# Kernel optimization log

Hardware: AMD Instinct MI355X
Metric: run time of the kernel (lower is better)

Reference implementation:

```python
import jax, jax.numpy as jnp
import numpy as np

B, S, D = 4, 2048, 512      # batch, seq_len, input_dim
E, H = 512, 8               # embed_dim, n_heads
HD = E // H                 # head_dim
ALPHA = 1.0                 # LRSA temperature


def setup_inputs() -> dict:
    key = jax.random.key(0)
    kx, kw1, kw2 = jax.random.split(key, 3)
    # xavier_uniform bounds for the two Linear layers (bias init is 0, as in module)
    b_qkv = float(np.sqrt(6.0 / (D + 3 * E)))
    b_o = float(np.sqrt(6.0 / (E + E)))
    return {
        "x": jax.random.normal(kx, (B, S, D), dtype=jnp.float32),
        "Wqkv": jax.random.uniform(kw1, (3 * E, D), jnp.float32, -b_qkv, b_qkv),
        "bqkv": jnp.zeros((3 * E,), jnp.float32),
        "Wo": jax.random.uniform(kw2, (E, E), jnp.float32, -b_o, b_o),
        "bo": jnp.zeros((E,), jnp.float32),
    }


def reference(x, Wqkv, bqkv, Wo, bo):
    Bx, Sx, _ = x.shape
    # QKV projection: [B,S,3E] -> [B,S,H,3*HD] -> [B,H,S,3*HD]
    qkv = (x @ Wqkv.T + bqkv).reshape(Bx, Sx, H, 3 * HD).transpose(0, 2, 1, 3)
    q, k, v = jnp.split(qkv, 3, axis=-1)  # each [B,H,S,HD]

    # LRSA: pairwise squared L2 distance logits ||q_i - k_j||^2
    q_norm2 = jnp.sum(q * q, axis=-1, keepdims=True)        # [B,H,S,1]
    k_norm2 = jnp.sum(k * k, axis=-1)[..., None, :]         # [B,H,1,S]
    qk = jnp.einsum("bhqd,bhkd->bhqk", q, k)                # [B,H,S,S]
    logits = q_norm2 - 2.0 * qk + k_norm2

    # global normalizers: frobenius norm of q, max per-token L2 norm of x
    fro_q = jnp.sqrt(jnp.sum(q * q))
    inf_2_x = jnp.max(jnp.sqrt(jnp.sum(x * x, axis=-1)))
    logits = logits / fro_q / inf_2_x

    attention = jax.nn.softmax(-ALPHA * logits, axis=-1)    # [B,H,S,S]
    values = jnp.einsum("bhqk,bhkd->bhqd", attention, v)    # [B,H,S,HD]
    values = values.transpose(0, 2, 1, 3).reshape(Bx, Sx, E)
    return values @ Wo.T + bo
```

## Files before the change

### kernel.cpp

```cpp
#include <hip/hip_runtime.h>
#include <hip/hip_bf16.h>
#include <math.h>

#define B_ 4
#define S_ 2048
#define D_ 512
#define E_ 512
#define H_ 8
#define HD_ 64
#define ALPHA_ 1.0f
#define M_ (B_*S_)
#define LOG2E_ 1.44269504088896340736f

typedef __attribute__((ext_vector_type(8))) short bf16x8;
typedef __attribute__((ext_vector_type(4))) float f32x4;

__device__ inline unsigned short f2bf(float f) {
    union { __hip_bfloat16 h; unsigned short u; } cv;
    cv.h = __float2bfloat16(f);
    return cv.u;
}
__device__ inline unsigned pack2bf(float a, float b) {
    union { __hip_bfloat162 h; unsigned u; } cv;
    cv.h = __float22bfloat162_rn(make_float2(a, b));
    return cv.u;
}
__device__ inline void gload16(const void* g, void* l) {
    __builtin_amdgcn_global_load_lds(
        (const __attribute__((address_space(1))) unsigned int*)g,
        (__attribute__((address_space(3))) unsigned int*)l, 16, 0, 0);
}
__device__ inline void gload4(const void* g, void* l) {
    __builtin_amdgcn_global_load_lds(
        (const __attribute__((address_space(1))) unsigned int*)g,
        (__attribute__((address_space(3))) unsigned int*)l, 4, 0, 0);
}

__global__ __launch_bounds__(256) void prep(const float* __restrict__ x,
                                            const float* __restrict__ Wqkv,
                                            const float* __restrict__ Wo,
                                            unsigned short* __restrict__ xbf,
                                            unsigned short* __restrict__ Wqkvb,
                                            unsigned short* __restrict__ Wob,
                                            float* __restrict__ xmax) {
    const int t   = threadIdx.x;
    const int bid = blockIdx.x;
    if (bid < 2048) {
        __shared__ float red[4];
        const int wid = t >> 6, lane = t & 63;
        const int row = bid * 4 + wid;
        const float* xr = &x[(size_t)row * D_ + lane * 8];
        const float4 a = *(const float4*)xr;
        const float4 b = *(const float4*)(xr + 4);
        float ss = a.x*a.x + a.y*a.y + a.z*a.z + a.w*a.w
                 + b.x*b.x + b.y*b.y + b.z*b.z + b.w*b.w;
        uint4 o;
        o.x = pack2bf(a.x, a.y); o.y = pack2bf(a.z, a.w);
        o.z = pack2bf(b.x, b.y); o.w = pack2bf(b.z, b.w);
        *(uint4*)&xbf[(size_t)row * D_ + lane * 8] = o;
        #pragma unroll
        for (int off = 32; off; off >>= 1) ss += __shfl_xor(ss, off);
        if (lane == 0) red[wid] = ss;
        __syncthreads();
        if (t == 0)
            xmax[bid] = fmaxf(fmaxf(red[0], red[1]), fmaxf(red[2], red[3]));
    } else {
        const int i  = (bid - 2048) * 256 + t;
        const int nq = 3 * E_ * D_ / 8;
        const float* src; unsigned short* dst; int j;
        if (i < nq) { src = Wqkv; dst = Wqkvb; j = i; }
        else        { src = Wo;   dst = Wob;   j = i - nq; }
        const float4 a = *(const float4*)&src[(size_t)j * 8];
        const float4 b = *(const float4*)&src[(size_t)j * 8 + 4];
        uint4 o;
        o.x = pack2bf(a.x, a.y); o.y = pack2bf(a.z, a.w);
        o.z = pack2bf(b.x, b.y); o.w = pack2bf(b.z, b.w);
        *(uint4*)&dst[(size_t)j * 8] = o;
    }
}

template<int N, int MODE>
__global__ __launch_bounds__(256) void gemm_mfma(const unsigned short* __restrict__ Abf,
                                                 const unsigned short* __restrict__ Wbf,
                                                 const float* __restrict__ bias,
                                                 void* __restrict__ out0,
                                                 void* __restrict__ out1,
                                                 void* __restrict__ out2,
                                                 float* __restrict__ part,
                                                 float* __restrict__ kn2) {
    __shared__ __align__(16) char At[16384];
    __shared__ __align__(16) char Wt[16384];

    const int t  = threadIdx.x;
    const int w  = t >> 6;
    const int l  = t & 63;
    const int g  = l >> 4;
    const int c  = l & 15;
    const int wm = w >> 1;
    const int wn = w & 1;
    const int m0 = blockIdx.y * 128;
    const int n0 = blockIdx.x * 128;

    f32x4 acc[4][4];
    #pragma unroll
    for (int i = 0; i < 4; ++i)
        #pragma unroll
        for (int j = 0; j < 4; ++j)
            #pragma unroll
            for (int r = 0; r < 4; ++r) acc[i][j][r] = 0.f;

    const int lr3 = l >> 3;
    const int colSwz = ((l & 7) * 16) ^ (lr3 << 4);
    const char* pA = (const char*)Abf + (size_t)(m0 + w * 8 + lr3) * 1024 + colSwz;
    const char* pB = (const char*)Wbf + (size_t)(n0 + w * 8 + lr3) * 1024 + colSwz;
    char* lA = At + w * 1024;
    char* lB = Wt + w * 1024;

    for (int k0 = 0; k0 < 512; k0 += 64) {
        __syncthreads();
        #pragma unroll
        for (int j = 0; j < 4; ++j) {
            gload16(pA + (size_t)j * 32768 + k0 * 2, lA + j * 4096);
            gload16(pB + (size_t)j * 32768 + k0 * 2, lB + j * 4096);
        }
        __syncthreads();

        bf16x8 af[4][2], wf[4][2];
        #pragma unroll
        for (int mt = 0; mt < 4; ++mt) {
            const int row = wm * 64 + mt * 16 + c;
            const int sw  = (row & 7) << 4;
            #pragma unroll
            for (int kc = 0; kc < 2; ++kc)
                af[mt][kc] = *(const bf16x8*)(At + row * 128 + (((kc * 4 + g) * 16) ^ sw));
        }
        #pragma unroll
        for (int nt = 0; nt < 4; ++nt) {
            const int row = wn * 64 + nt * 16 + c;
            const int sw  = (row & 7) << 4;
            #pragma unroll
            for (int kc = 0; kc < 2; ++kc)
                wf[nt][kc] = *(const bf16x8*)(Wt + row * 128 + (((kc * 4 + g) * 16) ^ sw));
        }
        #pragma unroll
        for (int mt = 0; mt < 4; ++mt)
            #pragma unroll
            for (int nt = 0; nt < 4; ++nt) {
                acc[mt][nt] = __builtin_amdgcn_mfma_f32_16x16x32_bf16(af[mt][0], wf[nt][0], acc[mt][nt], 0, 0, 0);
                acc[mt][nt] = __builtin_amdgcn_mfma_f32_16x16x32_bf16(af[mt][1], wf[nt][1], acc[mt][nt], 0, 0, 0);
            }
    }

    if (MODE == 1) {
        #pragma unroll
        for (int mt = 0; mt < 4; ++mt)
            #pragma unroll
            for (int reg = 0; reg < 4; ++reg) {
                const int m = m0 + wm * 64 + mt * 16 + g * 4 + reg;
                #pragma unroll
                for (int nt = 0; nt < 4; ++nt) {
                    const int n = n0 + wn * 64 + nt * 16 + c;
                    ((float*)out0)[(size_t)m * N + n] = acc[mt][nt][reg] + bias[n];
                }
            }
        return;
    }

    const int hb  = 2 * blockIdx.x + wn;
    const int cls = hb % 3;
    const int h   = hb / 3;
    const int b   = m0 >> 11;
    const int s0w = (m0 & 2047) + wm * 64;
    const size_t bhS = ((size_t)b * H_ + h) * S_;

    float kp[4][4];
    #pragma unroll
    for (int i = 0; i < 4; ++i)
        #pragma unroll
        for (int j = 0; j < 4; ++j) kp[i][j] = 0.f;

    if (cls == 2) {
        unsigned short* Vt_ = (unsigned short*)out2;
        #pragma unroll
        for (int nt = 0; nt < 4; ++nt) {
            const int n = n0 + wn * 64 + nt * 16 + c;
            const float bv = bias[n];
            const int d = nt * 16 + c;
            unsigned short* dbase = Vt_ + (((size_t)b * H_ + h) * HD_ + d) * S_ + s0w;
            #pragma unroll
            for (int mt = 0; mt < 4; ++mt) {
                uint2 pk;
                pk.x = pack2bf(acc[mt][nt][0] + bv, acc[mt][nt][1] + bv);
                pk.y = pack2bf(acc[mt][nt][2] + bv, acc[mt][nt][3] + bv);
                *(uint2*)&dbase[mt * 16 + g * 4] = pk;
            }
        }
    } else {
        unsigned short* dst0 = (cls == 0) ? (unsigned short*)out0 : (unsigned short*)out1;
        #pragma unroll
        for (int nt = 0; nt < 4; ++nt) {
            const int n = n0 + wn * 64 + nt * 16 + c;
            const float bv = bias[n];
            const int d = nt * 16 + c;
            #pragma unroll
            for (int mt = 0; mt < 4; ++mt)
                #pragma unroll
                for (int reg = 0; reg < 4; ++reg) {
                    const int s = s0w + mt * 16 + g * 4 + reg;
                    const float val = acc[mt][nt][reg] + bv;
                    kp[mt][reg] = fmaf(val, val, kp[mt][reg]);
                    dst0[(bhS + s) * HD_ + d] = f2bf(val);
                }
        }
    }

    __syncthreads();
    if (cls == 1) {
        float* scratch = (float*)At + wm * 1088;
        #pragma unroll
        for (int i = 0; i < 16; ++i) scratch[l * 17 + i] = kp[i >> 2][i & 3];
        asm volatile("s_waitcnt lgkmcnt(0)" ::: "memory");
        __builtin_amdgcn_sched_barrier(0);
        float sum = 0.f;
        #pragma unroll
        for (int cc = 0; cc < 16; ++cc)
            sum += scratch[(g * 16 + cc) * 17 + c];
        const int s = s0w + (c >> 2) * 16 + g * 4 + (c & 3);
        kn2[bhS + s] = sum;
    }
    __syncthreads();

    float qss = 0.f;
    if (cls == 0) {
        #pragma unroll
        for (int i = 0; i < 4; ++i)
            #pragma unroll
            for (int j = 0; j < 4; ++j) qss += kp[i][j];
    }
    float* red = (float*)At;
    red[t] = qss;
    __syncthreads();
    for (int s = 128; s; s >>= 1) {
        if (t < s) red[t] += red[t + s];
        __syncthreads();
    }
    if (t == 0) part[blockIdx.y * gridDim.x + blockIdx.x] = red[0];
}

__global__ __launch_bounds__(256) void finalize_scale(const float* __restrict__ part,
                                                      const float* __restrict__ xmax,
                                                      float* __restrict__ scal) {
    __shared__ float rs[256], rm[256];
    const int t = threadIdx.x;
    float ss = 0.f, mx = 0.f;
    for (int i = t; i < 768; i += 256) ss += part[i];
    for (int i = t; i < 2048; i += 256) mx = fmaxf(mx, xmax[i]);
    rs[t] = ss; rm[t] = mx;
    __syncthreads();
    for (int s = 128; s; s >>= 1) {
        if (t < s) { rs[t] += rs[t + s]; rm[t] = fmaxf(rm[t], rm[t + s]); }
        __syncthreads();
    }
    if (t == 0) scal[0] = ALPHA_ * LOG2E_ / (sqrtf(rs[0]) * sqrtf(rm[0]));
}

__global__ __launch_bounds__(512, 2) void attn_mfma(const unsigned short* __restrict__ Qb,
                                                    const unsigned short* __restrict__ Kb,
                                                    const unsigned short* __restrict__ Vtb,
                                                    const float* __restrict__ KN2,
                                                    const float* __restrict__ scal,
                                                    unsigned short* __restrict__ VALS) {
    __shared__ __align__(16) char lds[49664];
    char* Kl = lds;
    char* Vl = lds + 16384;
    char* Pl = lds + 32768;
    char* knl = lds + 49152;

    const int t  = threadIdx.x;
    const int w  = t >> 6;
    const int l  = t & 63;
    const int g  = l >> 4;
    const int c  = l & 15;
    const int bid  = blockIdx.y * gridDim.x + blockIdx.x;
    const int swid = (bid & 7) * 64 + (bid >> 3);
    const int bh = swid >> 4;
    const int qb = swid & 15;
    const float sc    = scal[0];
    const float ts2   = 2.0f * sc;
    const float nscal = -sc;

    const int qrow = qb * 128 + w * 16 + c;
    const size_t qoff = ((size_t)bh * S_ + qrow) * HD_;
    const bf16x8 qf0 = *(const bf16x8*)&Qb[qoff + g * 8];
    const bf16x8 qf1 = *(const bf16x8*)&Qb[qoff + 32 + g * 8];

    f32x4 acc[4];
    #pragma unroll
    for (int dt = 0; dt < 4; ++dt)
        #pragma unroll
        for (int r = 0; r < 4; ++r) acc[dt][r] = 0.f;
    float lpart = 0.f;

    const float* kn2g = &KN2[(size_t)bh * S_];
    char* Pw = Pl + w * 2048;
    const int swc = (c & 7) << 4;

    int offF[4][2];
    #pragma unroll
    for (int i = 0; i < 4; ++i) {
        offF[i][0] = (i * 16 + c) * 128 + ((g * 16) ^ swc);
        offF[i][1] = (i * 16 + c) * 128 + ((64 + g * 16) ^ swc);
    }
    int offPW[4];
    #pragma unroll
    for (int kt = 0; kt < 4; ++kt)
        offPW[kt] = c * 128 + ((kt * 32 + g * 8) ^ swc);
    const int offPA0 = c * 128 + ((g * 16) ^ swc);
    const int offPA1 = c * 128 + ((64 + g * 16) ^ swc);

    const int lr3 = l >> 3;
    const int colSwz = ((l & 7) * 16) ^ (lr3 << 4);
    const char* pK = (const char*)Kb + ((size_t)bh * S_ * HD_) * 2
                   + (size_t)(w * 8 + lr3) * 128 + colSwz;
    const char* pV = (const char*)Vtb + ((size_t)bh * HD_ * S_) * 2
                   + (size_t)(w * 8 + lr3) * (S_ * 2) + colSwz;
    char* lK = Kl + w * 1024;
    char* lV = Vl + w * 1024;

#define STAGE(T, buf) do {                                                    \
        gload16(pK + (size_t)(T) * 8192, lK + (buf) * 8192);                  \
        gload16(pV + (size_t)(T) * 128,  lV + (buf) * 8192);                  \
        if (w == 0) gload4(kn2g + (T) * 64 + l, knl + (buf) * 256);           \
    } while (0)

    auto compute_tile = [&](int cur) {
        const char* Kc = Kl + cur * 8192;
        const char* Vc = Vl + cur * 8192;
        const float* knc = (const float*)(knl + cur * 256);
        float sl[16];
        #pragma unroll
        for (int kt = 0; kt < 4; ++kt) {
            const bf16x8 ka0 = *(const bf16x8*)(Kc + offF[kt][0]);
            const bf16x8 ka1 = *(const bf16x8*)(Kc + offF[kt][1]);
            f32x4 sacc = {0.f, 0.f, 0.f, 0.f};
            sacc = __builtin_amdgcn_mfma_f32_16x16x32_bf16(ka0, qf0, sacc, 0, 0, 0);
            sacc = __builtin_amdgcn_mfma_f32_16x16x32_bf16(ka1, qf1, sacc, 0, 0, 0);
            const f32x4 kn4 = *(const f32x4*)&knc[kt * 16 + g * 4];
            #pragma unroll
            for (int rg = 0; rg < 4; ++rg)
                sl[kt * 4 + rg] = fmaf(sacc[rg], ts2, nscal * kn4[rg]);
        }

        float p[16];
        #pragma unroll
        for (int j = 0; j < 16; ++j) { p[j] = exp2f(sl[j]); lpart += p[j]; }

        #pragma unroll
        for (int kt = 0; kt < 4; ++kt) {
            uint2 pk;
            pk.x = pack2bf(p[kt * 4 + 0], p[kt * 4 + 1]);
            pk.y = pack2bf(p[kt * 4 + 2], p[kt * 4 + 3]);
            *(uint2*)(Pw + offPW[kt]) = pk;
        }
        asm volatile("s_waitcnt lgkmcnt(0)" ::: "memory");
        __builtin_amdgcn_sched_barrier(0);

        const bf16x8 pa0 = *(const bf16x8*)(Pw + offPA0);
        const bf16x8 pa1 = *(const bf16x8*)(Pw + offPA1);
        #pragma unroll
        for (int dt = 0; dt < 4; ++dt) {
            const bf16x8 vb0 = *(const bf16x8*)(Vc + offF[dt][0]);
            const bf16x8 vb1 = *(const bf16x8*)(Vc + offF[dt][1]);
            acc[dt] = __builtin_amdgcn_mfma_f32_16x16x32_bf16(pa0, vb0, acc[dt], 0, 0, 0);
            acc[dt] = __builtin_amdgcn_mfma_f32_16x16x32_bf16(pa1, vb1, acc[dt], 0, 0, 0);
        }
    };

    STAGE(0, 0);
    __syncthreads();
    for (int T = 0; T < 32; ++T) {
        const int cur = T & 1;
        if (T < 31) STAGE(T + 1, cur ^ 1);
        compute_tile(cur);
        __syncthreads();
    }
#undef STAGE

    lpart += __shfl_xor(lpart, 16);
    lpart += __shfl_xor(lpart, 32);

    const int b = bh >> 3, h = bh & 7;
    #pragma unroll
    for (int reg = 0; reg < 4; ++reg) {
        const float lq  = __shfl(lpart, g * 4 + reg);
        const float inv = 1.0f / lq;
        const int qg = qb * 128 + w * 16 + g * 4 + reg;
        unsigned short* dst = &VALS[((size_t)b * S_ + qg) * E_ + h * HD_];
        #pragma unroll
        for (int dt = 0; dt < 4; ++dt)
            dst[dt * 16 + c] = f2bf(acc[dt][reg] * inv);
    }
}

extern "C" void kernel_launch(void* const* d_in, const int* in_sizes, int n_in,
                              void* d_out, int out_size, void* d_ws, size_t ws_size,
                              hipStream_t stream) {
    const float* x    = (const float*)d_in[0];
    const float* Wqkv = (const float*)d_in[1];
    const float* bqkv = (const float*)d_in[2];
    const float* Wo   = (const float*)d_in[3];
    const float* bo   = (const float*)d_in[4];
    float* out = (float*)d_out;

    char* ws = (char*)d_ws;
    unsigned short* Qb    = (unsigned short*)(ws);
    unsigned short* Kb    = (unsigned short*)(ws + ((size_t) 8 << 20));
    unsigned short* Vtb   = (unsigned short*)(ws + ((size_t)16 << 20));
    unsigned short* VALb  = (unsigned short*)(ws + ((size_t)24 << 20));
    unsigned short* xbf   = (unsigned short*)(ws + ((size_t)32 << 20));
    unsigned short* Wqkvb = (unsigned short*)(ws + ((size_t)40 << 20));
    unsigned short* Wob   = (unsigned short*)(ws + ((size_t)42 << 20));
    float* KN2  = (float*)(ws + ((size_t)43 << 20));
    float* PART = (float*)(ws + ((size_t)43 << 20) + (256 << 10));
    float* XMAX = (float*)(ws + ((size_t)43 << 20) + (260 << 10));
    float* SCAL = (float*)(ws + ((size_t)43 << 20) + (272 << 10));

    prep<<<2560, 256, 0, stream>>>(x, Wqkv, Wo, xbf, Wqkvb, Wob, XMAX);

    gemm_mfma<3 * E_, 0><<<dim3(12, 64), 256, 0, stream>>>(xbf, Wqkvb, bqkv, Qb, Kb, Vtb, PART, KN2);

    finalize_scale<<<1, 256, 0, stream>>>(PART, XMAX, SCAL);

    attn_mfma<<<dim3(16, 32), 512, 0, stream>>>(Qb, Kb, Vtb, KN2, SCAL, VALb);

    gemm_mfma<E_, 1><<<dim3(4, 64), 256, 0, stream>>>(VALb, Wob, bo, out, nullptr, nullptr, nullptr, nullptr);
}
```

Before: 116.2 us.

## Double-buffer GEMM LDS tiles, fold scale finalize into attention, add MFMA priority

```diff
diff --git a/kernel.cpp b/kernel.cpp
--- a/kernel.cpp
+++ b/kernel.cpp
@@ -88,8 +88,8 @@
                                                  void* __restrict__ out2,
                                                  float* __restrict__ part,
                                                  float* __restrict__ kn2) {
-    __shared__ __align__(16) char At[16384];
-    __shared__ __align__(16) char Wt[16384];
+    __shared__ __align__(16) char At[2][16384];
+    __shared__ __align__(16) char Wt[2][16384];
 
     const int t  = threadIdx.x;
     const int w  = t >> 6;
@@ -113,17 +113,20 @@
     const int colSwz = ((l & 7) * 16) ^ (lr3 << 4);
     const char* pA = (const char*)Abf + (size_t)(m0 + w * 8 + lr3) * 1024 + colSwz;
     const char* pB = (const char*)Wbf + (size_t)(n0 + w * 8 + lr3) * 1024 + colSwz;
-    char* lA = At + w * 1024;
-    char* lB = Wt + w * 1024;
-
-    for (int k0 = 0; k0 < 512; k0 += 64) {
-        __syncthreads();
+
+    auto gstage = [&](int k0, int buf) {
         #pragma unroll
         for (int j = 0; j < 4; ++j) {
-            gload16(pA + (size_t)j * 32768 + k0 * 2, lA + j * 4096);
-            gload16(pB + (size_t)j * 32768 + k0 * 2, lB + j * 4096);
-        }
-        __syncthreads();
+            gload16(pA + (size_t)j * 32768 + (size_t)k0 * 2, At[buf] + w * 1024 + j * 4096);
+            gload16(pB + (size_t)j * 32768 + (size_t)k0 * 2, Wt[buf] + w * 1024 + j * 4096);
+        }
+    };
+
+    gstage(0, 0);
+    __syncthreads();
+    for (int i = 0; i < 8; ++i) {
+        const int buf = i & 1;
+        if (i < 7) gstage((i + 1) * 64, buf ^ 1);
 
         bf16x8 af[4][2], wf[4][2];
         #pragma unroll
@@ -132,7 +135,7 @@
             const int sw  = (row & 7) << 4;
             #pragma unroll
             for (int kc = 0; kc < 2; ++kc)
-                af[mt][kc] = *(const bf16x8*)(At + row * 128 + (((kc * 4 + g) * 16) ^ sw));
+                af[mt][kc] = *(const bf16x8*)(At[buf] + row * 128 + (((kc * 4 + g) * 16) ^ sw));
         }
         #pragma unroll
         for (int nt = 0; nt < 4; ++nt) {
@@ -140,8 +143,9 @@
             const int sw  = (row & 7) << 4;
             #pragma unroll
             for (int kc = 0; kc < 2; ++kc)
-                wf[nt][kc] = *(const bf16x8*)(Wt + row * 128 + (((kc * 4 + g) * 16) ^ sw));
-        }
+                wf[nt][kc] = *(const bf16x8*)(Wt[buf] + row * 128 + (((kc * 4 + g) * 16) ^ sw));
+        }
+        __builtin_amdgcn_s_setprio(1);
         #pragma unroll
         for (int mt = 0; mt < 4; ++mt)
             #pragma unroll
@@ -149,6 +153,8 @@
                 acc[mt][nt] = __builtin_amdgcn_mfma_f32_16x16x32_bf16(af[mt][0], wf[nt][0], acc[mt][nt], 0, 0, 0);
                 acc[mt][nt] = __builtin_amdgcn_mfma_f32_16x16x32_bf16(af[mt][1], wf[nt][1], acc[mt][nt], 0, 0, 0);
             }
+        __builtin_amdgcn_s_setprio(0);
+        __syncthreads();
     }
 
     if (MODE == 1) {
@@ -216,7 +222,7 @@
 
     __syncthreads();
     if (cls == 1) {
-        float* scratch = (float*)At + wm * 1088;
+        float* scratch = (float*)&At[0][0] + wm * 1088;
         #pragma unroll
         for (int i = 0; i < 16; ++i) scratch[l * 17 + i] = kp[i >> 2][i & 3];
         asm volatile("s_waitcnt lgkmcnt(0)" ::: "memory");
@@ -237,7 +243,7 @@
             #pragma unroll
             for (int j = 0; j < 4; ++j) qss += kp[i][j];
     }
-    float* red = (float*)At;
+    float* red = (float*)&At[0][0];
     red[t] = qss;
     __syncthreads();
     for (int s = 128; s; s >>= 1) {
@@ -247,28 +253,12 @@
     if (t == 0) part[blockIdx.y * gridDim.x + blockIdx.x] = red[0];
 }
 
-__global__ __launch_bounds__(256) void finalize_scale(const float* __restrict__ part,
-                                                      const float* __restrict__ xmax,
-                                                      float* __restrict__ scal) {
-    __shared__ float rs[256], rm[256];
-    const int t = threadIdx.x;
-    float ss = 0.f, mx = 0.f;
-    for (int i = t; i < 768; i += 256) ss += part[i];
-    for (int i = t; i < 2048; i += 256) mx = fmaxf(mx, xmax[i]);
-    rs[t] = ss; rm[t] = mx;
-    __syncthreads();
-    for (int s = 128; s; s >>= 1) {
-        if (t < s) { rs[t] += rs[t + s]; rm[t] = fmaxf(rm[t], rm[t + s]); }
-        __syncthreads();
-    }
-    if (t == 0) scal[0] = ALPHA_ * LOG2E_ / (sqrtf(rs[0]) * sqrtf(rm[0]));
-}
-
 __global__ __launch_bounds__(512, 2) void attn_mfma(const unsigned short* __restrict__ Qb,
                                                     const unsigned short* __restrict__ Kb,
                                                     const unsigned short* __restrict__ Vtb,
                                                     const float* __restrict__ KN2,
-                                                    const float* __restrict__ scal,
+                                                    const float* __restrict__ part,
+                                                    const float* __restrict__ xmax,
                                                     unsigned short* __restrict__ VALS) {
     __shared__ __align__(16) char lds[49664];
     char* Kl = lds;
@@ -285,7 +275,25 @@
     const int swid = (bid & 7) * 64 + (bid >> 3);
     const int bh = swid >> 4;
     const int qb = swid & 15;
-    const float sc    = scal[0];
+
+    float ss = 0.f, mx = 0.f;
+    for (int i = t; i < 768; i += 512) ss += part[i];
+    for (int i = t; i < 2048; i += 512) mx = fmaxf(mx, xmax[i]);
+    #pragma unroll
+    for (int off = 32; off; off >>= 1) {
+        ss += __shfl_xor(ss, off);
+        mx = fmaxf(mx, __shfl_xor(mx, off));
+    }
+    {
+        float* red = (float*)Pl;
+        if (l == 0) { red[w] = ss; red[8 + w] = mx; }
+        __syncthreads();
+        float tss = 0.f, tmx = 0.f;
+        #pragma unroll
+        for (int i = 0; i < 8; ++i) { tss += red[i]; tmx = fmaxf(tmx, red[8 + i]); }
+        ss = tss; mx = tmx;
+    }
+    const float sc    = ALPHA_ * LOG2E_ / (sqrtf(ss) * sqrtf(mx));
     const float ts2   = 2.0f * sc;
     const float nscal = -sc;
 
@@ -338,6 +346,7 @@
         const char* Vc = Vl + cur * 8192;
         const float* knc = (const float*)(knl + cur * 256);
         float sl[16];
+        __builtin_amdgcn_s_setprio(1);
         #pragma unroll
         for (int kt = 0; kt < 4; ++kt) {
             const bf16x8 ka0 = *(const bf16x8*)(Kc + offF[kt][0]);
@@ -350,6 +359,7 @@
             for (int rg = 0; rg < 4; ++rg)
                 sl[kt * 4 + rg] = fmaf(sacc[rg], ts2, nscal * kn4[rg]);
         }
+        __builtin_amdgcn_s_setprio(0);
 
         float p[16];
         #pragma unroll
@@ -367,6 +377,7 @@
 
         const bf16x8 pa0 = *(const bf16x8*)(Pw + offPA0);
         const bf16x8 pa1 = *(const bf16x8*)(Pw + offPA1);
+        __builtin_amdgcn_s_setprio(1);
         #pragma unroll
         for (int dt = 0; dt < 4; ++dt) {
             const bf16x8 vb0 = *(const bf16x8*)(Vc + offF[dt][0]);
@@ -374,6 +385,7 @@
             acc[dt] = __builtin_amdgcn_mfma_f32_16x16x32_bf16(pa0, vb0, acc[dt], 0, 0, 0);
             acc[dt] = __builtin_amdgcn_mfma_f32_16x16x32_bf16(pa1, vb1, acc[dt], 0, 0, 0);
         }
+        __builtin_amdgcn_s_setprio(0);
     };
 
     STAGE(0, 0);
@@ -423,15 +435,12 @@
     float* KN2  = (float*)(ws + ((size_t)43 << 20));
     float* PART = (float*)(ws + ((size_t)43 << 20) + (256 << 10));
     float* XMAX = (float*)(ws + ((size_t)43 << 20) + (260 << 10));
-    float* SCAL = (float*)(ws + ((size_t)43 << 20) + (272 << 10));
 
     prep<<<2560, 256, 0, stream>>>(x, Wqkv, Wo, xbf, Wqkvb, Wob, XMAX);
 
     gemm_mfma<3 * E_, 0><<<dim3(12, 64), 256, 0, stream>>>(xbf, Wqkvb, bqkv, Qb, Kb, Vtb, PART, KN2);
 
-    finalize_scale<<<1, 256, 0, stream>>>(PART, XMAX, SCAL);
-
-    attn_mfma<<<dim3(16, 32), 512, 0, stream>>>(Qb, Kb, Vtb, KN2, SCAL, VALb);
+    attn_mfma<<<dim3(16, 32), 512, 0, stream>>>(Qb, Kb, Vtb, KN2, PART, XMAX, VALb);
 
     gemm_mfma<E_, 1><<<dim3(4, 64), 256, 0, stream>>>(VALb, Wob, bo, out, nullptr, nullptr, nullptr, nullptr);
 }
```

New measurement: 113.1 us. 2.7% less time.
